# Kernel tuning notes

Hardware: AMD Instinct MI355X
Metric: run time of the kernel (lower is better)

Reference implementation:

```python
import jax, jax.numpy as jnp
import numpy as np

NTASKS = 10
CAP = 3          # semantic_cap_size / num_capsules
SEQ = 128        # max_seq_length / class_dim
HID = 768
ADAPT = 2048
NEG = -10000.0
NUM_ITERS = 3


def squash(t, axis=-1):
    sq = jnp.sum(t * t, axis=axis, keepdims=True)
    return (sq / (1.0 + sq)) * t / jnp.sqrt(sq)


def setup_inputs() -> dict:
    key = jax.random.key(0)
    ks = jax.random.split(key, 12)
    B = 128
    sc = 0.02
    return {
        "x": jax.random.normal(ks[0], (B, SEQ, HID), jnp.float32),
        "t": 5,
        "s": jnp.ones((1,), jnp.float32),
        "fc1_w": jax.random.normal(ks[1], (ADAPT, HID), jnp.float32) * sc,
        "fc1_b": jnp.zeros((ADAPT,), jnp.float32),
        "fc2_w": jax.random.normal(ks[2], (HID, ADAPT), jnp.float32) * sc,
        "fc2_b": jnp.zeros((HID,), jnp.float32),
        "efc1": jax.random.normal(ks[3], (NTASKS, ADAPT), jnp.float32),
        "efc2": jax.random.normal(ks[4], (NTASKS, HID), jnp.float32),
        "sfc1_w": jax.random.normal(ks[5], (NTASKS, 100, HID), jnp.float32) * sc,
        "sfc1_b": jnp.zeros((NTASKS, 100), jnp.float32),
        "sfc2_w": jax.random.normal(ks[6], (NTASKS, CAP, 100), jnp.float32) * sc,
        "sfc2_b": jnp.zeros((NTASKS, CAP), jnp.float32),
        "route_weights": jax.random.normal(ks[7], (CAP, NTASKS, SEQ * CAP, SEQ), jnp.float32),
        "larger_w": jax.random.normal(ks[8], (HID, CAP), jnp.float32) * sc,
        "larger_b": jnp.zeros((HID,), jnp.float32),
        "elarger": jax.random.normal(ks[9], (NTASKS, HID), jnp.float32),
    }


def reference(x, t, s, fc1_w, fc1_b, fc2_w, fc2_b, efc1, efc2,
              sfc1_w, sfc1_b, sfc2_w, sfc2_b, route_weights,
              larger_w, larger_b, elarger):
    B = x.shape[0]
    # ---- semantic capsules: per-task two-layer linear (no activation) ----
    h1 = jnp.einsum('blh,nkh->nblk', x, sfc1_w) + sfc1_b[:, None, None, :]     # [N,B,L,100]
    sem = jnp.einsum('nblk,nck->nblc', h1, sfc2_w) + sfc2_b[:, None, None, :]  # [N,B,L,C]
    # torch: cat of per-task views [B, L*C, 1] along last dim -> [B, L*C, N]
    sem = jnp.transpose(sem, (1, 2, 3, 0)).reshape(B, SEQ * CAP, NTASKS)
    sem = squash(sem, axis=-1)                 # squash over task axis
    sem = jnp.transpose(sem, (0, 2, 1))        # [B, N, L*C]

    # ---- tsv capsules: dynamic routing-by-agreement ----
    # priors[c,b,n,0,l] = sum_d sem[b,n,d] * route_weights[c,n,d,l]
    priors = jnp.einsum('bnd,cndl->cbnl', sem, route_weights)[:, :, :, None, :]  # [C,B,N,1,L]
    tsv = jnp.tril(jnp.ones((NTASKS, NTASKS), x.dtype))
    tsv_row = tsv[t].reshape(1, 1, NTASKS, 1, 1)                                  # [1,1,N,1,1]
    route_mask = jnp.where(tsv_row == 0, jnp.asarray(NEG, x.dtype), 0.0)

    logits = jnp.zeros_like(priors)
    vote_outputs = None
    for i in range(NUM_ITERS):
        logits = logits * tsv_row + route_mask
        probs = jax.nn.softmax(logits, axis=2)
        vote_outputs = jnp.sum(probs * priors, axis=2, keepdims=True)  # [C,B,1,1,L]
        outputs = squash(vote_outputs, axis=-1)
        if i != NUM_ITERS - 1:
            logits = logits + jnp.sum(priors * outputs, axis=-1, keepdims=True)

    # torch .view(B, L, -1) on contiguous [C,B,1,1,L] (row-major reshape)
    h_out = vote_outputs.reshape(B, SEQ, CAP)
    h_out = h_out @ larger_w.T + larger_b                       # [B,L,HID]
    glarger = jax.nn.sigmoid(s * elarger[t])                    # [HID]
    capsule_output = h_out * glarger

    # ---- masked adapter over (x + capsule_output) ----
    h = x + capsule_output
    gfc1 = jax.nn.sigmoid(s * efc1[t])
    gfc2 = jax.nn.sigmoid(s * efc2[t])
    h = jax.nn.relu(h @ fc1_w.T + fc1_b) * gfc1
    h = jax.nn.relu(h @ fc2_w.T + fc2_b) * gfc2
    return x + h
```

## Files before the change

### kernel.cpp

```cpp
#include <hip/hip_runtime.h>
#include <hip/hip_bf16.h>
#include <math.h>
#include <stdint.h>

typedef __bf16 bf16;
typedef __bf16 bf16x8 __attribute__((ext_vector_type(8)));
typedef __bf16 bf16x4 __attribute__((ext_vector_type(4)));
typedef float  f32x4  __attribute__((ext_vector_type(4)));

#define NTASKS 10
#define CAP    3
#define SEQ    128
#define HID    768
#define ADAPT  2048
#define BATCH  128
#define BL     (BATCH*SEQ)
#define NEGV   (-10000.0f)

__device__ __forceinline__ float sigmoidf_(float z) { return 1.f / (1.f + expf(-z)); }

__device__ __forceinline__ void gld16(const void* g, void* l) {
    auto gp = (const __attribute__((address_space(1))) uint32_t*)g;
    auto lp = (__attribute__((address_space(3))) uint32_t*)(uint32_t)(uintptr_t)l;
    __builtin_amdgcn_global_load_lds(gp, lp, 16, 0, 0);
}

__global__ void k_gates(const float* efc1, const float* efc2, const float* elarger,
                        const float* s, const int* tptr,
                        float* gfc1, float* gfc2, float* glarger) {
    int i = blockIdx.x * 256 + threadIdx.x;
    int t = *tptr; float sv = *s;
    if (i < ADAPT)                gfc1[i] = sigmoidf_(sv * efc1[t * ADAPT + i]);
    else if (i < ADAPT + HID)     { int j = i - ADAPT;        gfc2[j]    = sigmoidf_(sv * efc2[t * HID + j]); }
    else if (i < ADAPT + 2 * HID) { int j = i - ADAPT - HID;  glarger[j] = sigmoidf_(sv * elarger[t * HID + j]); }
}

__global__ void k_fusew(const float* sfc1_w, const float* sfc1_b,
                        const float* sfc2_w, const float* sfc2_b,
                        bf16* Wb, float* bb) {
    int j = blockIdx.x;
    int n = j / CAP;
    if (j >= 30) {
        for (int i = threadIdx.x; i < HID; i += 256) Wb[j * HID + i] = (bf16)0.f;
        if (threadIdx.x == 0) bb[j] = 0.f;
        return;
    }
    __shared__ float w2[100];
    if (threadIdx.x < 100) w2[threadIdx.x] = sfc2_w[j * 100 + threadIdx.x];
    __syncthreads();
    const float* w1 = sfc1_w + (size_t)n * 100 * HID;
    float a0 = 0, a1 = 0, a2 = 0;
    for (int k = 0; k < 100; ++k) {
        float s2 = w2[k];
        const float* r = w1 + k * HID;
        a0 += s2 * r[threadIdx.x];
        a1 += s2 * r[threadIdx.x + 256];
        a2 += s2 * r[threadIdx.x + 512];
    }
    Wb[j * HID + threadIdx.x]       = (bf16)a0;
    Wb[j * HID + threadIdx.x + 256] = (bf16)a1;
    Wb[j * HID + threadIdx.x + 512] = (bf16)a2;
    if (threadIdx.x == 0) {
        float b = sfc2_b[j];
        for (int k = 0; k < 100; ++k) b += sfc1_b[n * 100 + k] * w2[k];
        bb[j] = b;
    }
}

__global__ void k_convert(const float* fc1_w, const float* fc2_w, bf16* B1, bf16* B2) {
    int i = blockIdx.x * 256 + threadIdx.x;
    const int quarter = ADAPT * HID / 4;
    if (i < quarter) {
        float4 v = ((const float4*)fc1_w)[i];
        bf16x4 o = { (bf16)v.x, (bf16)v.y, (bf16)v.z, (bf16)v.w };
        ((bf16x4*)B1)[i] = o;
    } else if (i < 2 * quarter) {
        int j = i - quarter;
        float4 v = ((const float4*)fc2_w)[j];
        bf16x4 o = { (bf16)v.x, (bf16)v.y, (bf16)v.z, (bf16)v.w };
        ((bf16x4*)B2)[j] = o;
    }
}

__global__ void k_rwT(const float* __restrict__ rw, bf16* __restrict__ rwb) {
    int cn = blockIdx.x;
    int d0 = blockIdx.y * 64;
    __shared__ float t[64][129];
    const float* src = rw + (size_t)cn * 384 * 128;
    int tid = threadIdx.x;
    #pragma unroll
    for (int p = 0; p < 8; ++p) {
        int f4 = tid + p * 256;
        int row = f4 >> 5, c4 = (f4 & 31) * 4;
        float4 v = *(const float4*)(src + (size_t)(d0 + row) * 128 + c4);
        t[row][c4] = v.x; t[row][c4 + 1] = v.y; t[row][c4 + 2] = v.z; t[row][c4 + 3] = v.w;
    }
    __syncthreads();
    bf16* dst = rwb + (size_t)cn * 128 * 384 + d0;
    #pragma unroll
    for (int p = 0; p < 4; ++p) {
        int i8 = tid + p * 256;
        int l = i8 >> 3, d8 = (i8 & 7) * 8;
        bf16x8 o;
        #pragma unroll
        for (int i = 0; i < 8; ++i) o[i] = (bf16)t[d8 + i][l];
        *(bf16x8*)(dst + (size_t)l * 384 + d8) = o;
    }
}

__launch_bounds__(256)
__global__ void k_semg(const float* __restrict__ x, const bf16* __restrict__ Wb,
                       const float* __restrict__ bb, bf16* __restrict__ semb) {
    __shared__ __align__(16) bf16 As[64 * 32];
    __shared__ __align__(16) bf16 Bs[32 * 32];
    __shared__ float sem_s[64][33];
    const int tid = threadIdx.x;
    const int wave = tid >> 6, lane = tid & 63;
    const int tm = blockIdx.x;
    const int lr = lane & 15, kg = (lane >> 4) * 8;
    f32x4 acc[2] = {};

    const float* xbase = x + (size_t)(tm * 64 + (tid >> 2)) * HID + (tid & 3) * 8;
    const bf16* wbase = Wb + (size_t)(tid >> 2) * HID + (tid & 3) * 8;
    bf16* BsW = Bs + wave * 512;

    for (int k0 = 0; k0 < HID; k0 += 32) {
        float xv[8];
        *(float4*)&xv[0] = *(const float4*)(xbase + k0);
        *(float4*)&xv[4] = *(const float4*)(xbase + k0 + 4);
        __syncthreads();
        if (tid < 128) gld16(wbase + k0, BsW);
        bf16x8 xb;
        #pragma unroll
        for (int i = 0; i < 8; ++i) xb[i] = (bf16)xv[i];
        *(bf16x8*)&As[tid * 8] = xb;
        __syncthreads();
        bf16x8 af = *(const bf16x8*)&As[(wave * 16 + lr) * 32 + kg];
        bf16x8 b0 = *(const bf16x8*)&Bs[lr * 32 + kg];
        bf16x8 b1 = *(const bf16x8*)&Bs[(16 + lr) * 32 + kg];
        acc[0] = __builtin_amdgcn_mfma_f32_16x16x32_bf16(af, b0, acc[0], 0, 0, 0);
        acc[1] = __builtin_amdgcn_mfma_f32_16x16x32_bf16(af, b1, acc[1], 0, 0, 0);
    }

    #pragma unroll
    for (int n = 0; n < 2; ++n) {
        int col = n * 16 + lr;
        float bv = bb[col];
        #pragma unroll
        for (int r = 0; r < 4; ++r) {
            int row = wave * 16 + (lane >> 4) * 4 + r;
            sem_s[row][col] = acc[n][r] + bv;
        }
    }
    __syncthreads();
    if (tid < 64) {
        int bl = tm * 64 + tid;
        int b = bl >> 7, l = bl & 127;
        float vals[30];
        float sq[3] = {0.f, 0.f, 0.f};
        #pragma unroll
        for (int j = 0; j < 30; ++j) { float v = sem_s[tid][j]; vals[j] = v; sq[j % 3] += v * v; }
        float scl[3];
        #pragma unroll
        for (int c = 0; c < 3; ++c) scl[c] = (sq[c] / (1.f + sq[c])) / sqrtf(sq[c]);
        #pragma unroll
        for (int j = 0; j < 30; ++j)
            semb[((size_t)(j / 3) * BATCH + b) * 384 + l * 3 + (j % 3)] = (bf16)(vals[j] * scl[j % 3]);
    }
}

__launch_bounds__(256)
__global__ void k_priorsG(const bf16* __restrict__ semb, const bf16* __restrict__ rwb,
                          float* __restrict__ priors) {
    __shared__ __align__(16) bf16 As[128 * 32];
    __shared__ __align__(16) bf16 Bs[128 * 32];
    const int cn = blockIdx.x;
    const int c = cn / NTASKS, n = cn % NTASKS;
    const int tid = threadIdx.x;
    const int wave = tid >> 6, lane = tid & 63;
    const int wr = wave >> 1, wc = wave & 1;
    const int lr = lane & 15, kg = (lane >> 4) * 8;
    const int K = 384;
    f32x4 acc[4][4] = {};

    const bf16* Abase = semb + ((size_t)n * BATCH + (tid >> 2)) * K + (tid & 3) * 8;
    const bf16* Bbase = rwb + ((size_t)cn * 128 + (tid >> 2)) * K + (tid & 3) * 8;
    bf16* AsW = As + wave * 512;
    bf16* BsW = Bs + wave * 512;

    for (int k0 = 0; k0 < K; k0 += 32) {
        __syncthreads();
        gld16(Abase + k0, AsW);
        gld16(Abase + k0 + (size_t)64 * K, AsW + 2048);
        gld16(Bbase + k0, BsW);
        gld16(Bbase + k0 + (size_t)64 * K, BsW + 2048);
        __syncthreads();
        bf16x8 af[4], bfr[4];
        #pragma unroll
        for (int m = 0; m < 4; ++m)
            af[m] = *(const bf16x8*)&As[(wr * 64 + m * 16 + lr) * 32 + kg];
        #pragma unroll
        for (int nn = 0; nn < 4; ++nn)
            bfr[nn] = *(const bf16x8*)&Bs[(wc * 64 + nn * 16 + lr) * 32 + kg];
        #pragma unroll
        for (int m = 0; m < 4; ++m)
            #pragma unroll
            for (int nn = 0; nn < 4; ++nn)
                acc[m][nn] = __builtin_amdgcn_mfma_f32_16x16x32_bf16(af[m], bfr[nn], acc[m][nn], 0, 0, 0);
    }

    #pragma unroll
    for (int nn = 0; nn < 4; ++nn) {
        int col = wc * 64 + nn * 16 + lr;
        #pragma unroll
        for (int m = 0; m < 4; ++m) {
            int row0 = wr * 64 + m * 16 + (lane >> 4) * 4;
            #pragma unroll
            for (int r = 0; r < 4; ++r) {
                int row = row0 + r;
                priors[(((size_t)c * BATCH + row) * NTASKS + n) * 128 + col] = acc[m][nn][r];
            }
        }
    }
}

__global__ void k_routing(const float* __restrict__ priors, const int* tptr,
                          float* __restrict__ vote) {
    int cb = blockIdx.x;
    int lane = threadIdx.x;
    int t = *tptr;
    float p0[NTASKS], p1[NTASKS], ln[NTASKS];
    const float* pb = priors + (size_t)cb * NTASKS * 128;
    #pragma unroll
    for (int n = 0; n < NTASKS; ++n) {
        p0[n] = pb[n * 128 + lane];
        p1[n] = pb[n * 128 + 64 + lane];
        ln[n] = 0.f;
    }
    float v0 = 0.f, v1 = 0.f;
    for (int it = 0; it < 3; ++it) {
        float lm[NTASKS];
        float mx = -3.4e38f;
        #pragma unroll
        for (int n = 0; n < NTASKS; ++n) { lm[n] = (n <= t) ? ln[n] : NEGV; mx = fmaxf(mx, lm[n]); }
        float e[NTASKS], se = 0.f;
        #pragma unroll
        for (int n = 0; n < NTASKS; ++n) { e[n] = expf(lm[n] - mx); se += e[n]; }
        float inv = 1.f / se;
        v0 = 0.f; v1 = 0.f;
        #pragma unroll
        for (int n = 0; n < NTASKS; ++n) { float pr = e[n] * inv; v0 += pr * p0[n]; v1 += pr * p1[n]; }
        if (it == 2) break;
        float sq = v0 * v0 + v1 * v1;
        #pragma unroll
        for (int m = 32; m >= 1; m >>= 1) sq += __shfl_xor(sq, m);
        float scale = (sq / (1.f + sq)) / sqrtf(sq);
        float o0 = v0 * scale, o1 = v1 * scale;
        #pragma unroll
        for (int n = 0; n < NTASKS; ++n) {
            float d = p0[n] * o0 + p1[n] * o1;
            #pragma unroll
            for (int m = 32; m >= 1; m >>= 1) d += __shfl_xor(d, m);
            ln[n] = lm[n] + d;
        }
    }
    vote[(size_t)cb * 128 + lane]      = v0;
    vote[(size_t)cb * 128 + 64 + lane] = v1;
}

__global__ void k_buildH(const float* __restrict__ x, const float* __restrict__ vote,
                         const float* __restrict__ lw, const float* __restrict__ lb,
                         const float* __restrict__ glarger, bf16* __restrict__ H) {
    int idx = blockIdx.x * 256 + threadIdx.x;
    int bl = idx / 192, h4 = (idx % 192) * 4;
    float v0 = vote[bl * 3 + 0], v1 = vote[bl * 3 + 1], v2 = vote[bl * 3 + 2];
    float xa[4];
    *(float4*)xa = ((const float4*)x)[idx];
    bf16x4 o;
    #pragma unroll
    for (int r = 0; r < 4; ++r) {
        int hid = h4 + r;
        float hv = v0 * lw[hid * 3] + v1 * lw[hid * 3 + 1] + v2 * lw[hid * 3 + 2] + lb[hid];
        o[r] = (bf16)(xa[r] + hv * glarger[hid]);
    }
    ((bf16x4*)H)[idx] = o;
}

__device__ __forceinline__ void rd_a(const char* base, bf16x8 (&a)[4][2], int qr, int lr, int kq) {
    #pragma unroll
    for (int m = 0; m < 4; ++m)
        #pragma unroll
        for (int ks = 0; ks < 2; ++ks) {
            int row = qr * 64 + m * 16 + lr;
            a[m][ks] = *(const bf16x8*)(base + row * 128 + (((ks * 4 + kq) ^ (lr & 7)) << 4));
        }
}
__device__ __forceinline__ void rd_b(const char* base, bf16x8 (&b)[2][2], int qc, int lr, int kq) {
    #pragma unroll
    for (int n = 0; n < 2; ++n)
        #pragma unroll
        for (int ks = 0; ks < 2; ++ks) {
            int row = qc * 32 + n * 16 + lr;
            b[n][ks] = *(const bf16x8*)(base + row * 128 + (((ks * 4 + kq) ^ (lr & 7)) << 4));
        }
}
__device__ __forceinline__ void mm8(f32x4 (&acc)[8][4], bf16x8 (&a)[4][2], bf16x8 (&b)[2][2],
                                    int mh, int nh) {
    #pragma unroll
    for (int ks = 0; ks < 2; ++ks)
        #pragma unroll
        for (int m = 0; m < 4; ++m)
            #pragma unroll
            for (int n = 0; n < 2; ++n)
                acc[mh * 4 + m][nh * 2 + n] = __builtin_amdgcn_mfma_f32_16x16x32_bf16(
                    a[m][ks], b[n][ks], acc[mh * 4 + m][nh * 2 + n], 0, 0, 0);
}
__device__ __forceinline__ void phase_mid() {
    __builtin_amdgcn_s_barrier();
    asm volatile("s_waitcnt lgkmcnt(0)" ::: "memory");
    __builtin_amdgcn_sched_barrier(0);
    __builtin_amdgcn_s_setprio(1);
}
__device__ __forceinline__ void phase_end() {
    __builtin_amdgcn_s_setprio(0);
    __builtin_amdgcn_s_barrier();
}

template <int MODE>
__launch_bounds__(512, 2)
__global__ void k_gemm256(const bf16* __restrict__ A, const bf16* __restrict__ Bw,
                          const float* __restrict__ bias, const float* __restrict__ gate,
                          const float* __restrict__ X, void* __restrict__ Out,
                          int K, int N, int TN, int NT) {
    __shared__ __align__(16) char smem[131072];
    const int tid = threadIdx.x;
    const int lane = tid & 63, w = tid >> 6;
    const int lr = lane & 15, kq = lane >> 4;
    const int qr = w >> 2, qc = w & 3;
    int nwg = gridDim.x, bid = blockIdx.x;
    int wg = (bid & 7) * (nwg >> 3) + (bid >> 3);
    int tm = wg / TN, tn = wg % TN;

    const int r8  = w * 8 + (lane >> 3);
    const int sl8 = ((lane & 7) ^ ((lane >> 3) & 7)) * 8;
    auto stage = [&](const bf16* __restrict__ G, int grow0, int k0, char* slot) {
        const bf16* g0 = G + (size_t)(grow0 + r8) * K + k0 + sl8;
        gld16(g0, slot + w * 1024);
        gld16(g0 + (size_t)64 * K, slot + 8192 + w * 1024);
    };
    auto As_ = [&](int buf, int half) { return smem + ((buf * 2 + half) << 14); };
    auto Bs_ = [&](int buf, int half) { return smem + 65536 + ((buf * 2 + half) << 14); };

    f32x4 acc[8][4] = {};
    bf16x8 a[4][2], b[2][2];

    stage(A,  tm * 256,       0,  As_(0, 0));
    stage(Bw, tn * 256,       0,  Bs_(0, 0));
    stage(A,  tm * 256 + 128, 0,  As_(0, 1));
    stage(Bw, tn * 256 + 128, 0,  Bs_(0, 1));
    stage(A,  tm * 256,       64, As_(1, 0));
    stage(Bw, tn * 256 + 128, 64, Bs_(1, 1));
    asm volatile("s_waitcnt vmcnt(4)" ::: "memory");
    __builtin_amdgcn_s_barrier();

    for (int T = 0; T < NT; ++T) {
        const int buf = T & 1;
        const bool s1 = (T + 1 < NT), s2 = (T + 2 < NT);
        rd_a(As_(buf, 0), a, qr, lr, kq);
        rd_b(Bs_(buf, 0), b, qc, lr, kq);
        if (s1) stage(A, tm * 256 + 128, (T + 1) * 64, As_(buf ^ 1, 1));
        phase_mid(); mm8(acc, a, b, 0, 0); phase_end();
        rd_b(Bs_(buf, 1), b, qc, lr, kq);
        if (s1) stage(Bw, tn * 256, (T + 1) * 64, Bs_(buf ^ 1, 0));
        phase_mid(); mm8(acc, a, b, 0, 1); phase_end();
        rd_a(As_(buf, 1), a, qr, lr, kq);
        if (s2) stage(A, tm * 256, (T + 2) * 64, As_(buf, 0));
        phase_mid(); mm8(acc, a, b, 1, 1); phase_end();
        rd_b(Bs_(buf, 0), b, qc, lr, kq);
        if (s2) stage(Bw, tn * 256 + 128, (T + 2) * 64, Bs_(buf, 1));
        phase_mid(); mm8(acc, a, b, 1, 0);
        __builtin_amdgcn_s_setprio(0);
        if (s2) asm volatile("s_waitcnt vmcnt(4)" ::: "memory");
        else    asm volatile("s_waitcnt vmcnt(0)" ::: "memory");
        __builtin_amdgcn_s_barrier();
    }

    #pragma unroll
    for (int in = 0; in < 4; ++in) {
        int col = tn * 256 + (in >> 1) * 128 + qc * 32 + (in & 1) * 16 + lr;
        float bv = bias[col], gv = gate[col];
        #pragma unroll
        for (int im = 0; im < 8; ++im) {
            int row0 = tm * 256 + (im >> 2) * 128 + qr * 64 + (im & 3) * 16 + kq * 4;
            #pragma unroll
            for (int r = 0; r < 4; ++r) {
                float v = fmaxf(acc[im][in][r] + bv, 0.f) * gv;
                int row = row0 + r;
                if (MODE == 1) {
                    ((bf16*)Out)[(size_t)row * N + col] = (bf16)v;
                } else {
                    size_t o = (size_t)row * HID + col;
                    ((float*)Out)[o] = X[o] + v;
                }
            }
        }
    }
}

extern "C" void kernel_launch(void* const* d_in, const int* in_sizes, int n_in,
                              void* d_out, int out_size, void* d_ws, size_t ws_size,
                              hipStream_t stream) {
    const float* x      = (const float*)d_in[0];
    const int*   t      = (const int*)  d_in[1];
    const float* s      = (const float*)d_in[2];
    const float* fc1_w  = (const float*)d_in[3];
    const float* fc1_b  = (const float*)d_in[4];
    const float* fc2_w  = (const float*)d_in[5];
    const float* fc2_b  = (const float*)d_in[6];
    const float* efc1   = (const float*)d_in[7];
    const float* efc2   = (const float*)d_in[8];
    const float* sfc1_w = (const float*)d_in[9];
    const float* sfc1_b = (const float*)d_in[10];
    const float* sfc2_w = (const float*)d_in[11];
    const float* sfc2_b = (const float*)d_in[12];
    const float* rw     = (const float*)d_in[13];
    const float* lw     = (const float*)d_in[14];
    const float* lb     = (const float*)d_in[15];
    const float* elarger= (const float*)d_in[16];

    char* ws = (char*)d_ws;
    size_t off = 0;
    auto alloc = [&](size_t b) { void* p = ws + off; off = (off + b + 255) & ~(size_t)255; return p; };
    float* gfc1    = (float*)alloc(ADAPT * 4);
    float* gfc2    = (float*)alloc(HID * 4);
    float* glarger = (float*)alloc(HID * 4);
    bf16*  Wb      = (bf16*) alloc(32 * HID * 2);
    float* bb      = (float*)alloc(32 * 4);
    bf16*  B1      = (bf16*) alloc((size_t)ADAPT * HID * 2);
    bf16*  B2      = (bf16*) alloc((size_t)ADAPT * HID * 2);
    bf16*  semb    = (bf16*) alloc((size_t)NTASKS * BATCH * 384 * 2);
    bf16*  rwb     = (bf16*) alloc((size_t)30 * 128 * 384 * 2);
    float* priors  = (float*)alloc((size_t)CAP * BATCH * NTASKS * 128 * 4);
    float* vote    = (float*)alloc((size_t)CAP * BATCH * 128 * 4);
    bf16*  H1      = (bf16*) alloc((size_t)BL * ADAPT * 2);
    bf16*  H       = (bf16*)d_out;

    k_gates  <<<14, 256, 0, stream>>>(efc1, efc2, elarger, s, t, gfc1, gfc2, glarger);
    k_fusew  <<<32, 256, 0, stream>>>(sfc1_w, sfc1_b, sfc2_w, sfc2_b, Wb, bb);
    k_convert<<<3072, 256, 0, stream>>>(fc1_w, fc2_w, B1, B2);
    k_rwT    <<<dim3(30, 6), 256, 0, stream>>>(rw, rwb);
    k_semg   <<<BL / 64, 256, 0, stream>>>(x, Wb, bb, semb);
    k_priorsG<<<30, 256, 0, stream>>>(semb, rwb, priors);
    k_routing<<<CAP * BATCH, 64, 0, stream>>>(priors, t, vote);
    k_buildH <<<BL * 192 / 256, 256, 0, stream>>>(x, vote, lw, lb, glarger, H);
    k_gemm256<1><<<512, 512, 0, stream>>>(H,  B1, fc1_b, gfc1, nullptr, H1,   HID,   ADAPT, 8, HID / 64);
    k_gemm256<2><<<192, 512, 0, stream>>>(H1, B2, fc2_b, gfc2, x,       d_out, ADAPT, HID,  3, ADAPT / 64);
}
```

Baseline: 198.7 us.

## Replace 256x256 phased GEMM with 128x256 tile, K=32 double-buffered kernel

Result: no change. 199.0 us (+0.2%).

```diff
diff --git a/kernel.cpp b/kernel.cpp
--- a/kernel.cpp
+++ b/kernel.cpp
@@ -286,115 +286,78 @@
     ((bf16x4*)H)[idx] = o;
 }
 
-__device__ __forceinline__ void rd_a(const char* base, bf16x8 (&a)[4][2], int qr, int lr, int kq) {
-    #pragma unroll
-    for (int m = 0; m < 4; ++m)
-        #pragma unroll
-        for (int ks = 0; ks < 2; ++ks) {
-            int row = qr * 64 + m * 16 + lr;
-            a[m][ks] = *(const bf16x8*)(base + row * 128 + (((ks * 4 + kq) ^ (lr & 7)) << 4));
-        }
-}
-__device__ __forceinline__ void rd_b(const char* base, bf16x8 (&b)[2][2], int qc, int lr, int kq) {
-    #pragma unroll
-    for (int n = 0; n < 2; ++n)
-        #pragma unroll
-        for (int ks = 0; ks < 2; ++ks) {
-            int row = qc * 32 + n * 16 + lr;
-            b[n][ks] = *(const bf16x8*)(base + row * 128 + (((ks * 4 + kq) ^ (lr & 7)) << 4));
-        }
-}
-__device__ __forceinline__ void mm8(f32x4 (&acc)[8][4], bf16x8 (&a)[4][2], bf16x8 (&b)[2][2],
-                                    int mh, int nh) {
-    #pragma unroll
-    for (int ks = 0; ks < 2; ++ks)
-        #pragma unroll
-        for (int m = 0; m < 4; ++m)
-            #pragma unroll
-            for (int n = 0; n < 2; ++n)
-                acc[mh * 4 + m][nh * 2 + n] = __builtin_amdgcn_mfma_f32_16x16x32_bf16(
-                    a[m][ks], b[n][ks], acc[mh * 4 + m][nh * 2 + n], 0, 0, 0);
-}
-__device__ __forceinline__ void phase_mid() {
-    __builtin_amdgcn_s_barrier();
-    asm volatile("s_waitcnt lgkmcnt(0)" ::: "memory");
-    __builtin_amdgcn_sched_barrier(0);
-    __builtin_amdgcn_s_setprio(1);
-}
-__device__ __forceinline__ void phase_end() {
-    __builtin_amdgcn_s_setprio(0);
-    __builtin_amdgcn_s_barrier();
-}
-
 template <int MODE>
-__launch_bounds__(512, 2)
-__global__ void k_gemm256(const bf16* __restrict__ A, const bf16* __restrict__ Bw,
-                          const float* __restrict__ bias, const float* __restrict__ gate,
-                          const float* __restrict__ X, void* __restrict__ Out,
-                          int K, int N, int TN, int NT) {
-    __shared__ __align__(16) char smem[131072];
+__launch_bounds__(512, 4)
+__global__ void k_gemmW(const bf16* __restrict__ A, const bf16* __restrict__ Bw,
+                        const float* __restrict__ bias, const float* __restrict__ gate,
+                        const float* __restrict__ X, void* __restrict__ Out,
+                        int K, int N, int TN, int NT) {
+    __shared__ __align__(16) char smem[49152];
     const int tid = threadIdx.x;
     const int lane = tid & 63, w = tid >> 6;
     const int lr = lane & 15, kq = lane >> 4;
     const int qr = w >> 2, qc = w & 3;
-    int nwg = gridDim.x, bid = blockIdx.x;
-    int wg = (bid & 7) * (nwg >> 3) + (bid >> 3);
-    int tm = wg / TN, tn = wg % TN;
-
-    const int r8  = w * 8 + (lane >> 3);
-    const int sl8 = ((lane & 7) ^ ((lane >> 3) & 7)) * 8;
-    auto stage = [&](const bf16* __restrict__ G, int grow0, int k0, char* slot) {
-        const bf16* g0 = G + (size_t)(grow0 + r8) * K + k0 + sl8;
-        gld16(g0, slot + w * 1024);
-        gld16(g0 + (size_t)64 * K, slot + 8192 + w * 1024);
+    const int nwg = gridDim.x, bid = blockIdx.x;
+    const int cpx = nwg >> 3;
+    const int wg = (bid & 7) * cpx + (bid >> 3);
+    const int tm = wg / TN, tn = wg % TN;
+
+    const int srow = lane >> 2;
+    const int schunk = (lane & 3) ^ ((lane >> 3) & 3);
+    const bf16* Ab  = A  + (size_t)(tm * 128 + w * 16 + srow) * K + schunk * 8;
+    const bf16* Bb0 = Bw + (size_t)(tn * 256 + w * 16 + srow) * K + schunk * 8;
+    const bf16* Bb1 = Bb0 + (size_t)128 * K;
+    auto As_ = [&](int buf) { return smem + buf * 8192; };
+    auto Bs_ = [&](int buf) { return smem + 16384 + buf * 16384; };
+    auto stage = [&](int k0, int buf) {
+        gld16(Ab  + k0, As_(buf) + w * 1024);
+        gld16(Bb0 + k0, Bs_(buf) + w * 1024);
+        gld16(Bb1 + k0, Bs_(buf) + 8192 + w * 1024);
     };
-    auto As_ = [&](int buf, int half) { return smem + ((buf * 2 + half) << 14); };
-    auto Bs_ = [&](int buf, int half) { return smem + 65536 + ((buf * 2 + half) << 14); };
-
-    f32x4 acc[8][4] = {};
-    bf16x8 a[4][2], b[2][2];
-
-    stage(A,  tm * 256,       0,  As_(0, 0));
-    stage(Bw, tn * 256,       0,  Bs_(0, 0));
-    stage(A,  tm * 256 + 128, 0,  As_(0, 1));
-    stage(Bw, tn * 256 + 128, 0,  Bs_(0, 1));
-    stage(A,  tm * 256,       64, As_(1, 0));
-    stage(Bw, tn * 256 + 128, 64, Bs_(1, 1));
-    asm volatile("s_waitcnt vmcnt(4)" ::: "memory");
+
+    const int psw = (lr >> 1) & 3;
+    f32x4 acc[4][4] = {};
+    bf16x8 a[4], b[4];
+
+    stage(0, 0);
+    asm volatile("s_waitcnt vmcnt(0)" ::: "memory");
     __builtin_amdgcn_s_barrier();
 
     for (int T = 0; T < NT; ++T) {
         const int buf = T & 1;
-        const bool s1 = (T + 1 < NT), s2 = (T + 2 < NT);
-        rd_a(As_(buf, 0), a, qr, lr, kq);
-        rd_b(Bs_(buf, 0), b, qc, lr, kq);
-        if (s1) stage(A, tm * 256 + 128, (T + 1) * 64, As_(buf ^ 1, 1));
-        phase_mid(); mm8(acc, a, b, 0, 0); phase_end();
-        rd_b(Bs_(buf, 1), b, qc, lr, kq);
-        if (s1) stage(Bw, tn * 256, (T + 1) * 64, Bs_(buf ^ 1, 0));
-        phase_mid(); mm8(acc, a, b, 0, 1); phase_end();
-        rd_a(As_(buf, 1), a, qr, lr, kq);
-        if (s2) stage(A, tm * 256, (T + 2) * 64, As_(buf, 0));
-        phase_mid(); mm8(acc, a, b, 1, 1); phase_end();
-        rd_b(Bs_(buf, 0), b, qc, lr, kq);
-        if (s2) stage(Bw, tn * 256 + 128, (T + 2) * 64, Bs_(buf, 1));
-        phase_mid(); mm8(acc, a, b, 1, 0);
+        const bool more = (T + 1 < NT);
+        if (more) stage((T + 1) * 32, buf ^ 1);
+        const char* ab = As_(buf);
+        const char* bb = Bs_(buf);
+        #pragma unroll
+        for (int m = 0; m < 4; ++m)
+            a[m] = *(const bf16x8*)(ab + (qr * 64 + m * 16 + lr) * 64 + ((kq ^ psw) << 4));
+        #pragma unroll
+        for (int n = 0; n < 4; ++n)
+            b[n] = *(const bf16x8*)(bb + (qc * 64 + n * 16 + lr) * 64 + ((kq ^ psw) << 4));
+        asm volatile("s_waitcnt lgkmcnt(0)" ::: "memory");
+        __builtin_amdgcn_sched_barrier(0);
+        __builtin_amdgcn_s_setprio(1);
+        #pragma unroll
+        for (int m = 0; m < 4; ++m)
+            #pragma unroll
+            for (int n = 0; n < 4; ++n)
+                acc[m][n] = __builtin_amdgcn_mfma_f32_16x16x32_bf16(a[m], b[n], acc[m][n], 0, 0, 0);
         __builtin_amdgcn_s_setprio(0);
-        if (s2) asm volatile("s_waitcnt vmcnt(4)" ::: "memory");
-        else    asm volatile("s_waitcnt vmcnt(0)" ::: "memory");
+        if (more) asm volatile("s_waitcnt vmcnt(0)" ::: "memory");
         __builtin_amdgcn_s_barrier();
     }
 
     #pragma unroll
-    for (int in = 0; in < 4; ++in) {
-        int col = tn * 256 + (in >> 1) * 128 + qc * 32 + (in & 1) * 16 + lr;
+    for (int n = 0; n < 4; ++n) {
+        int col = tn * 256 + qc * 64 + n * 16 + lr;
         float bv = bias[col], gv = gate[col];
         #pragma unroll
-        for (int im = 0; im < 8; ++im) {
-            int row0 = tm * 256 + (im >> 2) * 128 + qr * 64 + (im & 3) * 16 + kq * 4;
+        for (int m = 0; m < 4; ++m) {
+            int row0 = tm * 128 + qr * 64 + m * 16 + kq * 4;
             #pragma unroll
             for (int r = 0; r < 4; ++r) {
-                float v = fmaxf(acc[im][in][r] + bv, 0.f) * gv;
+                float v = fmaxf(acc[m][n][r] + bv, 0.f) * gv;
                 int row = row0 + r;
                 if (MODE == 1) {
                     ((bf16*)Out)[(size_t)row * N + col] = (bf16)v;
@@ -453,6 +416,6 @@
     k_priorsG<<<30, 256, 0, stream>>>(semb, rwb, priors);
     k_routing<<<CAP * BATCH, 64, 0, stream>>>(priors, t, vote);
     k_buildH <<<BL * 192 / 256, 256, 0, stream>>>(x, vote, lw, lb, glarger, H);
-    k_gemm256<1><<<512, 512, 0, stream>>>(H,  B1, fc1_b, gfc1, nullptr, H1,   HID,   ADAPT, 8, HID / 64);
-    k_gemm256<2><<<192, 512, 0, stream>>>(H1, B2, fc2_b, gfc2, x,       d_out, ADAPT, HID,  3, ADAPT / 64);
-}
+    k_gemmW<1><<<1024, 512, 0, stream>>>(H,  B1, fc1_b, gfc1, nullptr, H1,   HID,   ADAPT, 8, HID / 32);
+    k_gemmW<2><<<384, 512, 0, stream>>>(H1, B2, fc2_b, gfc2, x,       d_out, ADAPT, HID,  3, ADAPT / 32);
+}
```
